# Kernel optimization log

Measured on AMD Instinct MI355X. Metric: run time of the kernel, lower is better.

## Reference

```python
import jax, jax.numpy as jnp
import numpy as np

B, T, D, H = 64, 1024, 256, 256


def _init_cell(key, input_size, hidden_size):
    K = 1.0 / np.sqrt(hidden_size)
    k1, k2, k3, k4 = jax.random.split(key, 4)
    u = lambda k, shape: jax.random.uniform(k, shape, jnp.float32, -K, K)
    return (u(k1, (3 * hidden_size, input_size)),  # w_ih
            u(k2, (3 * hidden_size, hidden_size)),  # w_hh
            u(k3, (3 * hidden_size,)),               # b_ih
            u(k4, (3 * hidden_size,)))               # b_hh


def setup_inputs() -> dict:
    key = jax.random.key(0)
    kx, kfw, kbw = jax.random.split(key, 3)
    x = jax.random.normal(kx, (B, T, D), dtype=jnp.float32)
    w_ih_fw, w_hh_fw, b_ih_fw, b_hh_fw = _init_cell(kfw, D, H)
    w_ih_bw, w_hh_bw, b_ih_bw, b_hh_bw = _init_cell(kbw, D, H)
    return {"x": x,
            "w_ih_fw": w_ih_fw, "w_hh_fw": w_hh_fw, "b_ih_fw": b_ih_fw, "b_hh_fw": b_hh_fw,
            "w_ih_bw": w_ih_bw, "w_hh_bw": w_hh_bw, "b_ih_bw": b_ih_bw, "b_hh_bw": b_hh_bw}


def _gru_direction(x, w_ih, w_hh, b_ih, b_hh, reverse):
    # Precompute the input-side GEMM for all timesteps at once: (B,T,3H)
    gates_x = jnp.einsum('btd,gd->btg', x, w_ih) + b_ih

    def step(h, gx):  # h: (B,H), gx: (B,3H)
        gh = h @ w_hh.T + b_hh
        rx, ux, mx = jnp.split(gx, 3, axis=-1)
        rh, uh, mh = jnp.split(gh, 3, axis=-1)
        r = jax.nn.sigmoid(rx + rh)
        z = jax.nn.sigmoid(ux + uh)
        n = jnp.tanh(mx + r * mh)
        h_new = z * h + (1.0 - z) * n
        return h_new, h_new

    h0 = jnp.zeros((x.shape[0], w_hh.shape[1]), x.dtype)
    xs = jnp.swapaxes(gates_x, 0, 1)  # (T,B,3H)
    h_last, ys = jax.lax.scan(step, h0, xs, reverse=reverse)
    return jnp.swapaxes(ys, 0, 1), h_last  # (B,T,H), (B,H)


def reference(x, w_ih_fw, w_hh_fw, b_ih_fw, b_hh_fw, w_ih_bw, w_hh_bw, b_ih_bw, b_hh_bw):
    outputs_fw, h_fw = _gru_direction(x, w_ih_fw, w_hh_fw, b_ih_fw, b_hh_fw, reverse=False)
    outputs_bw, h_bw = _gru_direction(x, w_ih_bw, w_hh_bw, b_ih_bw, b_hh_bw, reverse=True)
    outputs = jnp.concatenate((outputs_fw, outputs_bw), axis=-1)  # (B,T,2H)
    return outputs, h_fw, h_bw
```

## Files before the change

kernel.cpp:

```cpp
#include <hip/hip_runtime.h>
#include <hip/hip_fp16.h>

typedef unsigned int u32;
typedef _Float16 half2_t __attribute__((ext_vector_type(2)));
typedef u32 u32x4 __attribute__((ext_vector_type(4)));

#define NB   64
#define NT   1024
#define NH   256
#define G3   768
#define NK2  128
#define WPACK_ELEMS 98304
#define KSPLIT 4
#define KPER   32

#define PIN(x) asm volatile("" : "+v"(x))

static __device__ __forceinline__ float fdot2f(u32 a, u32 b, float c) {
#if __has_builtin(__builtin_amdgcn_fdot2)
    return __builtin_amdgcn_fdot2(__builtin_bit_cast(half2_t, a),
                                  __builtin_bit_cast(half2_t, b), c, false);
#else
    half2_t av = __builtin_bit_cast(half2_t, a);
    half2_t bv = __builtin_bit_cast(half2_t, b);
    c = fmaf((float)av[0], (float)bv[0], c);
    c = fmaf((float)av[1], (float)bv[1], c);
    return c;
#endif
}

static __device__ __forceinline__ u32 packh2(float lo, float hi) {
    half2_t v;
    v[0] = (_Float16)lo;
    v[1] = (_Float16)hi;
    return __builtin_bit_cast(u32, v);
}

static __device__ __forceinline__ float sigmoidf_fast(float x) {
    return 1.0f / (1.0f + __expf(-x));
}
static __device__ __forceinline__ float tanhf_fast(float x) {
    return 2.0f / (1.0f + __expf(-2.0f * x)) - 1.0f;
}

__global__ void pack_w(const float* __restrict__ src_fw,
                       const float* __restrict__ src_bw,
                       u32* __restrict__ dst) {
    int id = blockIdx.x * 256 + threadIdx.x;
    int dir = id >= WPACK_ELEMS;
    int r   = id - dir * WPACK_ELEMS;
    int j    = r & 255;
    int q    = r >> 8;
    int gate = q % 3;
    int k2   = q / 3;
    const float* src = dir ? src_bw : src_fw;
    int g = gate * 256 + j;
    float lo = src[g * 256 + 2 * k2];
    float hi = src[g * 256 + 2 * k2 + 1];
    dst[dir * WPACK_ELEMS + k2 * G3 + g] = packh2(lo, hi);
}

__global__ __launch_bounds__(256) void gemm_gx(
        const float* __restrict__ x, const u32* __restrict__ wihp,
        const float* __restrict__ bih_fw, const float* __restrict__ bih_bw,
        const float* __restrict__ bhh_fw, const float* __restrict__ bhh_bw,
        _Float16* __restrict__ gx) {
    int dir = blockIdx.y;
    int m0  = blockIdx.x * 16;
    int j   = threadIdx.x;

    __shared__ u32 xs[16][NK2];
    #pragma unroll
    for (int rep = 0; rep < 8; ++rep) {
        int lin = rep * 256 + j;
        int mi  = lin >> 7;
        int k2  = lin & 127;
        const float* xr = x + (size_t)(m0 + mi) * 256 + 2 * k2;
        xs[mi][k2] = packh2(xr[0], xr[1]);
    }
    __syncthreads();

    const u32* wp = wihp + dir * WPACK_ELEMS;
    const float* bih = dir ? bih_bw : bih_fw;
    const float* bhh = dir ? bhh_bw : bhh_fw;

    float accr[16], accz[16], accn[16];
    #pragma unroll
    for (int mi = 0; mi < 16; ++mi) { accr[mi] = 0.f; accz[mi] = 0.f; accn[mi] = 0.f; }

    #pragma unroll 2
    for (int k2 = 0; k2 < NK2; ++k2) {
        u32 wr = wp[k2 * G3 + j];
        u32 wz = wp[k2 * G3 + 256 + j];
        u32 wn = wp[k2 * G3 + 512 + j];
        #pragma unroll
        for (int mi = 0; mi < 16; ++mi) {
            u32 xv = xs[mi][k2];
            accr[mi] = fdot2f(xv, wr, accr[mi]);
            accz[mi] = fdot2f(xv, wz, accz[mi]);
            accn[mi] = fdot2f(xv, wn, accn[mi]);
        }
    }

    float br = bih[j] + bhh[j];
    float bz = bih[256 + j] + bhh[256 + j];
    float bn = bih[512 + j];
    _Float16* gxd = gx + (size_t)dir * 65536 * G3;
    #pragma unroll
    for (int mi = 0; mi < 16; ++mi) {
        size_t row = (size_t)(m0 + mi) * G3;
        gxd[row + j]       = (_Float16)(accr[mi] + br);
        gxd[row + 256 + j] = (_Float16)(accz[mi] + bz);
        gxd[row + 512 + j] = (_Float16)(accn[mi] + bn);
    }
}

__global__ __launch_bounds__(1024)
__attribute__((amdgpu_waves_per_eu(4, 4)))
void gru_rec(
        const _Float16* __restrict__ gx, const u32* __restrict__ whhp,
        const float* __restrict__ bhh_fw, const float* __restrict__ bhh_bw,
        float* __restrict__ out) {
    int b   = blockIdx.x;
    int dir = blockIdx.y;
    int tid = threadIdx.x;
    int j   = tid & 255;
    int q   = tid >> 8;

    __shared__ alignas(16) u32 hl[2][NK2];
    __shared__ float psum[KSPLIT - 1][G3];
    __shared__ char occ_pad[86016];
    if (gx == nullptr) occ_pad[tid] = 1;

    const u32* wp = whhp + dir * WPACK_ELEMS;

    u32 wr[KPER], wz[KPER], wn[KPER];
    #pragma unroll
    for (int k = 0; k < KPER; ++k) {
        int k2 = q * KPER + k;
        wr[k] = wp[k2 * G3 + j];       PIN(wr[k]);
        wz[k] = wp[k2 * G3 + 256 + j]; PIN(wz[k]);
        wn[k] = wp[k2 * G3 + 512 + j]; PIN(wn[k]);
    }

    const float* bhh = dir ? bhh_bw : bhh_fw;
    float bhn = bhh[512 + j];

    const _Float16* gxp = gx + ((size_t)dir * NB + b) * NT * G3;
    float* outp = out + (size_t)b * NT * 512 + dir * 256 + j;

    float h = 0.0f;
    if (tid < 256) ((_Float16*)hl)[tid] = (_Float16)0.0f;
    __syncthreads();

    const int tstep = dir ? -1 : 1;
    int t = dir ? (NT - 1) : 0;

    _Float16 ngr = (_Float16)0.f, ngz = (_Float16)0.f, ngn = (_Float16)0.f;
    if (q == 0) {
        const _Float16* gxt = gxp + (size_t)t * G3;
        ngr = gxt[j]; ngz = gxt[256 + j]; ngn = gxt[512 + j];
    }

    int cur = 0;
    for (int tt = 0; tt < NT; ++tt, t += tstep) {
        float gxr = (float)ngr, gxz = (float)ngz, gxn = (float)ngn;
        if (q == 0 && tt + 1 < NT) {
            const _Float16* gxt = gxp + (size_t)(t + tstep) * G3;
            ngr = gxt[j]; ngz = gxt[256 + j]; ngn = gxt[512 + j];
        }

        float ar = 0.f, az = 0.f, an = 0.f;
        const u32x4* hp = (const u32x4*)hl[cur] + q * 8;
        #pragma unroll
        for (int k4 = 0; k4 < 8; ++k4) {
            u32x4 hv = hp[k4];
            #pragma unroll
            for (int e = 0; e < 4; ++e) {
                int k = k4 * 4 + e;
                ar = fdot2f(hv[e], wr[k], ar);
                az = fdot2f(hv[e], wz[k], az);
                an = fdot2f(hv[e], wn[k], an);
            }
        }
        if (q != 0) {
            psum[q - 1][j]       = ar;
            psum[q - 1][256 + j] = az;
            psum[q - 1][512 + j] = an;
        }

        asm volatile("s_waitcnt lgkmcnt(0)" ::: "memory");
        __builtin_amdgcn_s_barrier();
        asm volatile("" ::: "memory");

        if (q == 0) {
            float arT = ar + psum[0][j]       + psum[1][j]       + psum[2][j];
            float azT = az + psum[0][256 + j] + psum[1][256 + j] + psum[2][256 + j];
            float anT = an + psum[0][512 + j] + psum[1][512 + j] + psum[2][512 + j];

            float r = sigmoidf_fast(gxr + arT);
            float z = sigmoidf_fast(gxz + azT);
            float n = tanhf_fast(gxn + r * (anT + bhn));
            h = z * h + (1.0f - z) * n;

            ((_Float16*)hl[cur ^ 1])[j] = (_Float16)h;
            outp[(size_t)t * 512] = h;
        }

        asm volatile("s_waitcnt lgkmcnt(0)" ::: "memory");
        __builtin_amdgcn_s_barrier();
        asm volatile("" ::: "memory");
        cur ^= 1;
    }

    if (q == 0) {
        float* hout = out + (size_t)NB * NT * 512 + dir * (NB * NH);
        hout[b * NH + j] = h;
    }
}

extern "C" void kernel_launch(void* const* d_in, const int* in_sizes, int n_in,
                              void* d_out, int out_size, void* d_ws, size_t ws_size,
                              hipStream_t stream) {
    const float* x      = (const float*)d_in[0];
    const float* wih_fw = (const float*)d_in[1];
    const float* whh_fw = (const float*)d_in[2];
    const float* bih_fw = (const float*)d_in[3];
    const float* bhh_fw = (const float*)d_in[4];
    const float* wih_bw = (const float*)d_in[5];
    const float* whh_bw = (const float*)d_in[6];
    const float* bih_bw = (const float*)d_in[7];
    const float* bhh_bw = (const float*)d_in[8];
    float* out = (float*)d_out;

    char* ws = (char*)d_ws;
    _Float16* gx = (_Float16*)ws;
    u32* wihp = (u32*)(ws + 201326592);
    u32* whhp = (u32*)(ws + 202113024);

    pack_w<<<768, 256, 0, stream>>>(wih_fw, wih_bw, wihp);
    pack_w<<<768, 256, 0, stream>>>(whh_fw, whh_bw, whhp);
    gemm_gx<<<dim3(4096, 2), 256, 0, stream>>>(x, wihp, bih_fw, bih_bw,
                                               bhh_fw, bhh_bw, gx);
    gru_rec<<<dim3(NB, 2), 1024, 0, stream>>>(gx, whhp, bhh_fw, bhh_bw, out);
}
```

Baseline: 1.666 ms.

## Halve recurrent block to 512 threads with 2-way K split and deeper gx prefetch

The recurrent GRU kernel now uses 512 threads per block, with each thread holding 64 packed fp16 weight pairs per gate instead of 32. This reduces the cross-thread partial-sum reduction from four slices to two and cuts barrier participants per step. The gate-input prefetch is deepened to two timesteps ahead to hide global load latency. In exchange, each thread does twice the serial dot-product work per step and holds 192 weight registers, which raises register pressure and risks spills. The LDS occupancy pad is resized to keep one block per CU.

```diff
diff --git a/kernel.cpp b/kernel.cpp
--- a/kernel.cpp
+++ b/kernel.cpp
@@ -11,8 +11,7 @@
 #define G3   768
 #define NK2  128
 #define WPACK_ELEMS 98304
-#define KSPLIT 4
-#define KPER   32
+#define KPER   64
 
 #define PIN(x) asm volatile("" : "+v"(x))
 
@@ -115,8 +114,7 @@
     }
 }
 
-__global__ __launch_bounds__(1024)
-__attribute__((amdgpu_waves_per_eu(4, 4)))
+__global__ __launch_bounds__(512)
 void gru_rec(
         const _Float16* __restrict__ gx, const u32* __restrict__ whhp,
         const float* __restrict__ bhh_fw, const float* __restrict__ bhh_bw,
@@ -128,9 +126,13 @@
     int q   = tid >> 8;
 
     __shared__ alignas(16) u32 hl[2][NK2];
-    __shared__ float psum[KSPLIT - 1][G3];
-    __shared__ char occ_pad[86016];
-    if (gx == nullptr) occ_pad[tid] = 1;
+    __shared__ float psum[G3];
+    __shared__ u32 occ_pad[21504];
+    if (blockIdx.x == 0x7FFFFFFFu) {
+        occ_pad[(tid * 21u) % 21504u] = tid;
+        __syncthreads();
+        out[tid] = (float)occ_pad[(tid * 7u) % 21504u];
+    }
 
     const u32* wp = whhp + dir * WPACK_ELEMS;
 
@@ -156,24 +158,28 @@
     const int tstep = dir ? -1 : 1;
     int t = dir ? (NT - 1) : 0;
 
-    _Float16 ngr = (_Float16)0.f, ngz = (_Float16)0.f, ngn = (_Float16)0.f;
+    _Float16 g0r = (_Float16)0.f, g0z = (_Float16)0.f, g0n = (_Float16)0.f;
+    _Float16 g1r = (_Float16)0.f, g1z = (_Float16)0.f, g1n = (_Float16)0.f;
     if (q == 0) {
         const _Float16* gxt = gxp + (size_t)t * G3;
-        ngr = gxt[j]; ngz = gxt[256 + j]; ngn = gxt[512 + j];
+        g0r = gxt[j]; g0z = gxt[256 + j]; g0n = gxt[512 + j];
+        const _Float16* gxt1 = gxp + (size_t)(t + tstep) * G3;
+        g1r = gxt1[j]; g1z = gxt1[256 + j]; g1n = gxt1[512 + j];
     }
 
     int cur = 0;
     for (int tt = 0; tt < NT; ++tt, t += tstep) {
-        float gxr = (float)ngr, gxz = (float)ngz, gxn = (float)ngn;
-        if (q == 0 && tt + 1 < NT) {
-            const _Float16* gxt = gxp + (size_t)(t + tstep) * G3;
-            ngr = gxt[j]; ngz = gxt[256 + j]; ngn = gxt[512 + j];
+        float gxr = (float)g0r, gxz = (float)g0z, gxn = (float)g0n;
+        g0r = g1r; g0z = g1z; g0n = g1n;
+        if (q == 0 && tt + 2 < NT) {
+            const _Float16* gxt = gxp + (size_t)(t + 2 * tstep) * G3;
+            g1r = gxt[j]; g1z = gxt[256 + j]; g1n = gxt[512 + j];
         }
 
         float ar = 0.f, az = 0.f, an = 0.f;
-        const u32x4* hp = (const u32x4*)hl[cur] + q * 8;
+        const u32x4* hp = (const u32x4*)hl[cur] + q * 16;
         #pragma unroll
-        for (int k4 = 0; k4 < 8; ++k4) {
+        for (int k4 = 0; k4 < 16; ++k4) {
             u32x4 hv = hp[k4];
             #pragma unroll
             for (int e = 0; e < 4; ++e) {
@@ -184,9 +190,9 @@
             }
         }
         if (q != 0) {
-            psum[q - 1][j]       = ar;
-            psum[q - 1][256 + j] = az;
-            psum[q - 1][512 + j] = an;
+            psum[j]       = ar;
+            psum[256 + j] = az;
+            psum[512 + j] = an;
         }
 
         asm volatile("s_waitcnt lgkmcnt(0)" ::: "memory");
@@ -194,9 +200,9 @@
         asm volatile("" ::: "memory");
 
         if (q == 0) {
-            float arT = ar + psum[0][j]       + psum[1][j]       + psum[2][j];
-            float azT = az + psum[0][256 + j] + psum[1][256 + j] + psum[2][256 + j];
-            float anT = an + psum[0][512 + j] + psum[1][512 + j] + psum[2][512 + j];
+            float arT = ar + psum[j];
+            float azT = az + psum[256 + j];
+            float anT = an + psum[512 + j];
 
             float r = sigmoidf_fast(gxr + arT);
             float z = sigmoidf_fast(gxz + azT);
@@ -242,5 +248,5 @@
     pack_w<<<768, 256, 0, stream>>>(whh_fw, whh_bw, whhp);
     gemm_gx<<<dim3(4096, 2), 256, 0, stream>>>(x, wihp, bih_fw, bih_bw,
                                                bhh_fw, bhh_bw, gx);
-    gru_rec<<<dim3(NB, 2), 1024, 0, stream>>>(gx, whhp, bhh_fw, bhh_bw, out);
-}
+    gru_rec<<<dim3(NB, 2), 512, 0, stream>>>(gx, whhp, bhh_fw, bhh_bw, out);
+}
```

New measurement: 1.635 ms. Within noise of the previous version (-1.9%).
